# Performance work log

Measured on AMD Instinct MI355X. Metric: run time of the kernel, lower is better.

The kernel has to match this reference:

```python
import jax, jax.numpy as jnp
import numpy as np

N_EDGES = 1_600_000
N_NODES = 100_000
IN_CH = 32
OUT_CH = 64
TOTAL_DIM = IN_CH * 4 * 3  # 4 aggregators x 3 scalers


def setup_inputs() -> dict:
    key = jax.random.key(0)
    k1, k2, k3, k4 = jax.random.split(key, 4)
    messages = jax.random.normal(k1, (N_EDGES, IN_CH), dtype=jnp.float32)
    dst = jax.random.randint(k2, (N_EDGES,), 0, N_NODES, dtype=jnp.int64)
    W = jax.random.normal(k3, (OUT_CH, TOTAL_DIM), dtype=jnp.float32) / np.sqrt(TOTAL_DIM)
    b = jax.random.normal(k4, (OUT_CH,), dtype=jnp.float32) * 0.01
    return {"messages": messages, "dst": dst, "num_nodes": N_NODES, "W": W, "b": b}


def reference(messages, dst, num_nodes, W, b):
    # degree (clamped to >=1, matching scatter_count)
    ones = jnp.ones(dst.shape[0], dtype=messages.dtype)
    deg_raw = jax.ops.segment_sum(ones, dst, num_segments=num_nodes)
    deg = jnp.maximum(deg_raw, 1.0)

    # mean
    s = jax.ops.segment_sum(messages, dst, num_segments=num_nodes)  # [N, d]
    mean = s / deg[:, None]

    # max / min with empty-segment -> 0 (torch fills -inf/+inf then zeroes)
    mx = jax.ops.segment_max(messages, dst, num_segments=num_nodes)
    mx = jnp.where(jnp.isneginf(mx), jnp.zeros_like(mx), mx)
    mn = jax.ops.segment_min(messages, dst, num_segments=num_nodes)
    mn = jnp.where(jnp.isposinf(mn), jnp.zeros_like(mn), mn)

    # std: mean of squared deviations from per-node mean
    sq_diff = (messages - mean[dst]) ** 2
    var = jax.ops.segment_sum(sq_diff, dst, num_segments=num_nodes) / deg[:, None]
    std = jnp.sqrt(var + 1e-8)

    amp = jnp.log(deg + 1.0)[:, None]       # amplification scaler
    att = (1.0 / (deg + 1.0))[:, None]      # attenuation scaler

    results = []
    for agg in (mean, mx, mn, std):  # order matches default aggregators
        results.extend([agg, agg * amp, agg * att])  # identity, amp, att
    combined = jnp.concatenate(results, axis=-1)  # [N, 12*d]
    return combined @ W.T + b
```

## Files before the change

kernel.cpp:

```cpp
#include <hip/hip_runtime.h>
#include <math.h>

#define NE 1600000
#define NN 100000
#define NBKT 391
#define BINCH 8192
#define NBINBLK ((NE + BINCH - 1) / BINCH)

typedef __attribute__((ext_vector_type(8))) short bf16x8;
typedef __attribute__((ext_vector_type(4))) float f32x4;

static __device__ inline short f2bf(float f) {
  unsigned u = __float_as_uint(f);
  u += 0x7FFFu + ((u >> 16) & 1u);
  return (short)(u >> 16);
}

__global__ void k_init0(int* __restrict__ bktcnt) {
  int t = threadIdx.x;
  if (t < NBKT) bktcnt[t] = 0;
}

__global__ void k_wprep(const float* __restrict__ W, short* __restrict__ Wf) {
  int j = blockIdx.x * 256 + threadIdx.x;
  if (j < 12 * 4 * 64 * 8) {
    int i = j & 7, l = (j >> 3) & 63, ct = (j >> 9) & 3, kt = j >> 11;
    int col = ct * 16 + (l & 15);
    int k = kt * 32 + (l >> 4) * 8 + i;
    Wf[j] = f2bf(W[col * 384 + k]);
  }
}

__global__ __launch_bounds__(256) void k_bktcount(const int* __restrict__ dst,
                                                  int* __restrict__ bktcnt) {
  __shared__ int hist[NBKT];
  int t = threadIdx.x;
  for (int j = t; j < NBKT; j += 256) hist[j] = 0;
  __syncthreads();
  int start = blockIdx.x * BINCH;
  int lim = min(BINCH, NE - start);
  for (int j = t; j < lim; j += 256) atomicAdd(&hist[dst[start + j] >> 8], 1);
  __syncthreads();
  for (int j = t; j < NBKT; j += 256) {
    int h = hist[j];
    if (h) atomicAdd(&bktcnt[j], h);
  }
}

__global__ void k_bktscan(const int* __restrict__ bktcnt, int* __restrict__ bktoff,
                          int* __restrict__ bkcur, int* __restrict__ off) {
  __shared__ int s[512];
  int t = threadIdx.x;
  int v = (t < NBKT) ? bktcnt[t] : 0;
  s[t] = v;
  __syncthreads();
  for (int d = 1; d < 512; d <<= 1) {
    int x = (t >= d) ? s[t - d] : 0;
    __syncthreads();
    s[t] += x;
    __syncthreads();
  }
  if (t < NBKT) {
    int ex = s[t] - v;
    bktoff[t] = ex;
    bkcur[t] = ex;
  }
  if (t == 0) {
    bktoff[NBKT] = NE;
    off[NN] = NE;
  }
}

__global__ __launch_bounds__(256) void k_bin(const int* __restrict__ dst,
                                             int* __restrict__ bkcur,
                                             int2* __restrict__ pairs) {
  __shared__ int sdst[BINCH];
  __shared__ int hist[NBKT];
  int t = threadIdx.x;
  int start = blockIdx.x * BINCH;
  int lim = min(BINCH, NE - start);
  for (int j = t; j < NBKT; j += 256) hist[j] = 0;
  __syncthreads();
  for (int j = t; j < lim; j += 256) {
    int d = dst[start + j];
    sdst[j] = d;
    atomicAdd(&hist[d >> 8], 1);
  }
  __syncthreads();
  for (int j = t; j < NBKT; j += 256) {
    int h = hist[j];
    hist[j] = h ? atomicAdd(&bkcur[j], h) : 0;
  }
  __syncthreads();
  for (int j = t; j < lim; j += 256) {
    int d = sdst[j];
    int q = atomicAdd(&hist[d >> 8], 1);
    pairs[q] = make_int2(d, start + j);
  }
}

__global__ __launch_bounds__(256) void k_build(const int2* __restrict__ pairs,
                                               const int* __restrict__ bktoff,
                                               int* __restrict__ off,
                                               int* __restrict__ eid) {
  __shared__ int cnt[256];
  __shared__ int loc[256];
  int b = blockIdx.x, t = threadIdx.x;
  int base = bktoff[b];
  int m = bktoff[b + 1] - base;
  cnt[t] = 0;
  __syncthreads();
  for (int i = t; i < m; i += 256) atomicAdd(&cnt[pairs[base + i].x & 255], 1);
  __syncthreads();
  int v = cnt[t];
  loc[t] = v;
  __syncthreads();
  for (int d = 1; d < 256; d <<= 1) {
    int x = (t >= d) ? loc[t - d] : 0;
    __syncthreads();
    loc[t] += x;
    __syncthreads();
  }
  int ex = base + loc[t] - v;
  int node = b * 256 + t;
  if (node < NN) off[node] = ex;
  __syncthreads();
  loc[t] = ex;
  __syncthreads();
  for (int i = t; i < m; i += 256) {
    int2 pe = pairs[base + i];
    int p = atomicAdd(&loc[pe.x & 255], 1);
    eid[p] = pe.y;
  }
}

__global__ __launch_bounds__(256, 6) void k_fused(const float* __restrict__ msg,
                                                  const int* __restrict__ off,
                                                  const int* __restrict__ eid,
                                                  const short* __restrict__ Wf,
                                                  const float* __restrict__ bias,
                                                  float* __restrict__ out) {
  int wid = threadIdx.x >> 6, lane = threadIdx.x & 63;
  int r = lane & 15, oct = lane >> 4;
  int nb = (blockIdx.x * 4 + wid) * 16;
  if (nb >= NN) return;
  int node = nb + r;

  int e0 = off[node], e1 = off[node + 1];

  float sv[8], qv[8], xv[8], nv[8];
#pragma unroll
  for (int i = 0; i < 8; i++) {
    sv[i] = 0.f;
    qv[i] = 0.f;
    xv[i] = -INFINITY;
    nv[i] = INFINITY;
  }

  const float* mbase = msg + oct * 8;
  int p = e0;
  int nfull = (e1 - e0) >> 2;
  int ea0 = 0, ea1 = 0, ea2 = 0, ea3 = 0;
  if (nfull > 0) {
    ea0 = eid[p];
    ea1 = eid[p + 1];
    ea2 = eid[p + 2];
    ea3 = eid[p + 3];
  }
  for (int it = 0; it < nfull; ++it) {
    int c0 = ea0, c1 = ea1, c2 = ea2, c3 = ea3;
    p += 4;
    if (it + 1 < nfull) {
      ea0 = eid[p];
      ea1 = eid[p + 1];
      ea2 = eid[p + 2];
      ea3 = eid[p + 3];
    }
    const f32x4* r0 = (const f32x4*)(mbase + (size_t)c0 * 32);
    const f32x4* r1 = (const f32x4*)(mbase + (size_t)c1 * 32);
    const f32x4* r2 = (const f32x4*)(mbase + (size_t)c2 * 32);
    const f32x4* r3 = (const f32x4*)(mbase + (size_t)c3 * 32);
    f32x4 va0 = r0[0], vb0 = r0[1];
    f32x4 va1 = r1[0], vb1 = r1[1];
    f32x4 va2 = r2[0], vb2 = r2[1];
    f32x4 va3 = r3[0], vb3 = r3[1];
#pragma unroll
    for (int i = 0; i < 4; i++) {
      float w0 = va0[i], w1 = va1[i], w2 = va2[i], w3 = va3[i];
      sv[i] += w0 + w1 + w2 + w3;
      qv[i] += w0 * w0 + w1 * w1 + w2 * w2 + w3 * w3;
      xv[i] = fmaxf(fmaxf(xv[i], fmaxf(w0, w1)), fmaxf(w2, w3));
      nv[i] = fminf(fminf(nv[i], fminf(w0, w1)), fminf(w2, w3));
      float z0 = vb0[i], z1 = vb1[i], z2 = vb2[i], z3 = vb3[i];
      sv[i + 4] += z0 + z1 + z2 + z3;
      qv[i + 4] += z0 * z0 + z1 * z1 + z2 * z2 + z3 * z3;
      xv[i + 4] = fmaxf(fmaxf(xv[i + 4], fmaxf(z0, z1)), fmaxf(z2, z3));
      nv[i + 4] = fminf(fminf(nv[i + 4], fminf(z0, z1)), fminf(z2, z3));
    }
  }
  for (; p < e1; ++p) {
    int e = eid[p];
    const f32x4* rp = (const f32x4*)(mbase + (size_t)e * 32);
    f32x4 a = rp[0], b = rp[1];
#pragma unroll
    for (int i = 0; i < 4; i++) {
      float v0 = a[i], v1 = b[i];
      sv[i] += v0;
      qv[i] += v0 * v0;
      xv[i] = fmaxf(xv[i], v0);
      nv[i] = fminf(nv[i], v0);
      sv[i + 4] += v1;
      qv[i + 4] += v1 * v1;
      xv[i + 4] = fmaxf(xv[i + 4], v1);
      nv[i + 4] = fminf(nv[i + 4], v1);
    }
  }

  float degr = (float)(e1 - e0);
  float deg = fmaxf(degr, 1.f);
  float inv = 1.f / deg;
  float amp = logf(deg + 1.f);
  float att = 1.f / (deg + 1.f);

#pragma unroll
  for (int i = 0; i < 8; i++) {
    float me = sv[i] * inv;
    float va = fmaxf(qv[i] * inv - me * me, 0.f);
    sv[i] = me;
    qv[i] = sqrtf(va + 1e-8f);
    xv[i] = (xv[i] == -INFINITY) ? 0.f : xv[i];
    nv[i] = (nv[i] == INFINITY) ? 0.f : nv[i];
  }

  f32x4 acc[4] = {{0.f, 0.f, 0.f, 0.f},
                  {0.f, 0.f, 0.f, 0.f},
                  {0.f, 0.f, 0.f, 0.f},
                  {0.f, 0.f, 0.f, 0.f}};
  float scal[3] = {1.f, amp, att};
  const bf16x8* Bp = (const bf16x8*)Wf;
#pragma unroll
  for (int kt = 0; kt < 12; kt++) {
    const float* ag = (kt < 3) ? sv : (kt < 6) ? xv : (kt < 9) ? nv : qv;
    float sc = scal[kt % 3];
    bf16x8 b0 = Bp[(kt * 4 + 0) * 64 + lane];
    bf16x8 b1 = Bp[(kt * 4 + 1) * 64 + lane];
    bf16x8 b2 = Bp[(kt * 4 + 2) * 64 + lane];
    bf16x8 b3 = Bp[(kt * 4 + 3) * 64 + lane];
    bf16x8 af;
#pragma unroll
    for (int i = 0; i < 8; i++) af[i] = f2bf(ag[i] * sc);
    acc[0] = __builtin_amdgcn_mfma_f32_16x16x32_bf16(af, b0, acc[0], 0, 0, 0);
    acc[1] = __builtin_amdgcn_mfma_f32_16x16x32_bf16(af, b1, acc[1], 0, 0, 0);
    acc[2] = __builtin_amdgcn_mfma_f32_16x16x32_bf16(af, b2, acc[2], 0, 0, 0);
    acc[3] = __builtin_amdgcn_mfma_f32_16x16x32_bf16(af, b3, acc[3], 0, 0, 0);
    __builtin_amdgcn_sched_barrier(0);
  }

#pragma unroll
  for (int ct = 0; ct < 4; ct++) {
    int ocol = ct * 16 + r;
    float bb = bias[ocol];
#pragma unroll
    for (int j = 0; j < 4; j++) {
      int orow = nb + oct * 4 + j;
      out[orow * 64 + ocol] = acc[ct][j] + bb;
    }
  }
}

extern "C" void kernel_launch(void* const* d_in, const int* in_sizes, int n_in,
                              void* d_out, int out_size, void* d_ws, size_t ws_size,
                              hipStream_t stream) {
  const float* msg = (const float*)d_in[0];
  const int* dst = (const int*)d_in[1];
  const float* W = (const float*)d_in[3];
  const float* bias = (const float*)d_in[4];
  float* out = (float*)d_out;

  int* wsi = (int*)d_ws;
  int2* pairs = (int2*)wsi;
  int* eid = wsi + 2 * NE;
  int* off = wsi + 3 * NE;
  int* bktcnt = wsi + 3 * NE + NN + 1;
  int* bktoff = bktcnt + NBKT;
  int* bkcur = bktoff + NBKT + 1;
  short* Wfrag = (short*)(bkcur + NBKT);

  k_init0<<<1, 512, 0, stream>>>(bktcnt);
  k_wprep<<<96, 256, 0, stream>>>(W, Wfrag);
  k_bktcount<<<NBINBLK, 256, 0, stream>>>(dst, bktcnt);
  k_bktscan<<<1, 512, 0, stream>>>(bktcnt, bktoff, bkcur, off);
  k_bin<<<NBINBLK, 256, 0, stream>>>(dst, bkcur, pairs);
  k_build<<<NBKT, 256, 0, stream>>>(pairs, bktoff, off, eid);
  k_fused<<<(NN / 16 + 3) / 4, 256, 0, stream>>>(msg, off, eid, Wfrag, bias, out);
}
```

Measured before the change: 128.5 us.

## Permute messages into a per-node contiguous bf16 buffer before aggregation

Adds a new path, used when the workspace is large enough. It builds CSR offsets with per-node atomic counting and a two-pass scan. It then scatters every message row into a destination-sorted buffer packed as bf16, so the fused aggregation kernel streams contiguous rows instead of gathering through an edge-id indirection. This is meant to remove the random-gather latency and the eid loads in the fused kernel. In exchange it adds a full write and re-read of a 100MB permuted copy with scattered writes, and it rounds messages to bf16 before computing the mean, std, max and min. The old bucket-sort path is kept as a fallback for small workspaces.

```diff
diff --git a/kernel.cpp b/kernel.cpp
--- a/kernel.cpp
+++ b/kernel.cpp
@@ -3,12 +3,14 @@
 
 #define NE 1600000
 #define NN 100000
+#define NBLK ((NN + 255) / 256)
 #define NBKT 391
 #define BINCH 8192
 #define NBINBLK ((NE + BINCH - 1) / BINCH)
 
 typedef __attribute__((ext_vector_type(8))) short bf16x8;
 typedef __attribute__((ext_vector_type(4))) float f32x4;
+typedef __attribute__((ext_vector_type(4))) unsigned int u32x4;
 
 static __device__ inline short f2bf(float f) {
   unsigned u = __float_as_uint(f);
@@ -16,10 +18,11 @@
   return (short)(u >> 16);
 }
 
-__global__ void k_init0(int* __restrict__ bktcnt) {
-  int t = threadIdx.x;
-  if (t < NBKT) bktcnt[t] = 0;
-}
+static __device__ inline void unpack2(unsigned int u, float& lo, float& hi) {
+  lo = __uint_as_float(u << 16);
+  hi = __uint_as_float(u & 0xffff0000u);
+}
+
 
 __global__ void k_wprep(const float* __restrict__ W, short* __restrict__ Wf) {
   int j = blockIdx.x * 256 + threadIdx.x;
@@ -29,6 +32,209 @@
     int k = kt * 32 + (l >> 4) * 8 + i;
     Wf[j] = f2bf(W[col * 384 + k]);
   }
+}
+
+__global__ void k_zero(int* __restrict__ cnt) {
+  int i = blockIdx.x * 256 + threadIdx.x;
+  if (i < NN) cnt[i] = 0;
+}
+
+__global__ void k_count(const int* __restrict__ dst, int* __restrict__ cnt) {
+  int e = (blockIdx.x * 256 + threadIdx.x) * 4;
+  if (e + 4 <= NE) {
+    int4 d4 = *(const int4*)(dst + e);
+    atomicAdd(&cnt[d4.x], 1);
+    atomicAdd(&cnt[d4.y], 1);
+    atomicAdd(&cnt[d4.z], 1);
+    atomicAdd(&cnt[d4.w], 1);
+  } else {
+    for (; e < NE; ++e) atomicAdd(&cnt[dst[e]], 1);
+  }
+}
+
+__global__ void k_scan1(const int* __restrict__ cnt, int* __restrict__ bsum) {
+  __shared__ int s[256];
+  int t = threadIdx.x, i = blockIdx.x * 256 + t;
+  s[t] = (i < NN) ? cnt[i] : 0;
+  __syncthreads();
+  for (int d = 128; d > 0; d >>= 1) {
+    if (t < d) s[t] += s[t + d];
+    __syncthreads();
+  }
+  if (t == 0) bsum[blockIdx.x] = s[0];
+}
+
+__global__ void k_scan3(const int* __restrict__ cnt, const int* __restrict__ bsum,
+                        int* __restrict__ off, int* __restrict__ cur) {
+  __shared__ int pre[256];
+  __shared__ int s[256];
+  int t = threadIdx.x, b = blockIdx.x, i = b * 256 + t;
+  int a = 0;
+  for (int j = t; j < b; j += 256) a += bsum[j];
+  pre[t] = a;
+  __syncthreads();
+  for (int d = 128; d > 0; d >>= 1) {
+    if (t < d) pre[t] += pre[t + d];
+    __syncthreads();
+  }
+  int base = pre[0];
+  int v = (i < NN) ? cnt[i] : 0;
+  s[t] = v;
+  __syncthreads();
+  for (int d = 1; d < 256; d <<= 1) {
+    int x = (t >= d) ? s[t - d] : 0;
+    __syncthreads();
+    s[t] += x;
+    __syncthreads();
+  }
+  int ex = s[t] - v + base;
+  if (i < NN) {
+    off[i] = ex;
+    cur[i] = ex;
+  }
+  if (i == NN - 1) off[NN] = ex + v;
+}
+
+
+__global__ __launch_bounds__(256) void k_perm(const float* __restrict__ msg,
+                                              const int* __restrict__ dst,
+                                              int* __restrict__ cur,
+                                              unsigned int* __restrict__ pm) {
+  int gid = blockIdx.x * 256 + threadIdx.x;
+  int e = gid >> 3, q = gid & 7;
+  f32x4 v = *(const f32x4*)(msg + (size_t)gid * 4);
+  int lane = threadIdx.x & 63;
+  int p = 0;
+  if ((lane & 7) == 0) p = atomicAdd(&cur[dst[e]], 1);
+  p = __shfl(p, lane & 56);
+  unsigned int u0 =
+      (unsigned int)(unsigned short)f2bf(v[0]) | ((unsigned int)(unsigned short)f2bf(v[1]) << 16);
+  unsigned int u1 =
+      (unsigned int)(unsigned short)f2bf(v[2]) | ((unsigned int)(unsigned short)f2bf(v[3]) << 16);
+  *(uint2*)((char*)pm + (size_t)p * 64 + q * 8) = make_uint2(u0, u1);
+}
+
+__global__ __launch_bounds__(256, 6) void k_fused(const unsigned int* __restrict__ pm,
+                                                  const int* __restrict__ off,
+                                                  const short* __restrict__ Wf,
+                                                  const float* __restrict__ bias,
+                                                  float* __restrict__ out) {
+  int wid = threadIdx.x >> 6, lane = threadIdx.x & 63;
+  int r = lane & 15, oct = lane >> 4;
+  int nb = (blockIdx.x * 4 + wid) * 16;
+  if (nb >= NN) return;
+  int node = nb + r;
+
+  int e0 = off[node], e1 = off[node + 1];
+
+  float sv[8], qv[8], xv[8], nv[8];
+#pragma unroll
+  for (int i = 0; i < 8; i++) {
+    sv[i] = 0.f;
+    qv[i] = 0.f;
+    xv[i] = -INFINITY;
+    nv[i] = INFINITY;
+  }
+
+  int p = e0;
+  int nfull = (e1 - e0) >> 2;
+  for (int it = 0; it < nfull; ++it, p += 4) {
+    u32x4 U0 = *(const u32x4*)(pm + (size_t)p * 16 + oct * 4);
+    u32x4 U1 = *(const u32x4*)(pm + (size_t)(p + 1) * 16 + oct * 4);
+    u32x4 U2 = *(const u32x4*)(pm + (size_t)(p + 2) * 16 + oct * 4);
+    u32x4 U3 = *(const u32x4*)(pm + (size_t)(p + 3) * 16 + oct * 4);
+#pragma unroll
+    for (int j = 0; j < 4; j++) {
+      float a0, b0, a1, b1, a2, b2, a3, b3;
+      unpack2(U0[j], a0, b0);
+      unpack2(U1[j], a1, b1);
+      unpack2(U2[j], a2, b2);
+      unpack2(U3[j], a3, b3);
+      int i0 = 2 * j, i1 = 2 * j + 1;
+      sv[i0] += a0 + a1 + a2 + a3;
+      qv[i0] += a0 * a0 + a1 * a1 + a2 * a2 + a3 * a3;
+      xv[i0] = fmaxf(fmaxf(xv[i0], fmaxf(a0, a1)), fmaxf(a2, a3));
+      nv[i0] = fminf(fminf(nv[i0], fminf(a0, a1)), fminf(a2, a3));
+      sv[i1] += b0 + b1 + b2 + b3;
+      qv[i1] += b0 * b0 + b1 * b1 + b2 * b2 + b3 * b3;
+      xv[i1] = fmaxf(fmaxf(xv[i1], fmaxf(b0, b1)), fmaxf(b2, b3));
+      nv[i1] = fminf(fminf(nv[i1], fminf(b0, b1)), fminf(b2, b3));
+    }
+  }
+  for (; p < e1; ++p) {
+    u32x4 U = *(const u32x4*)(pm + (size_t)p * 16 + oct * 4);
+#pragma unroll
+    for (int j = 0; j < 4; j++) {
+      float a, b;
+      unpack2(U[j], a, b);
+      int i0 = 2 * j, i1 = 2 * j + 1;
+      sv[i0] += a;
+      qv[i0] += a * a;
+      xv[i0] = fmaxf(xv[i0], a);
+      nv[i0] = fminf(nv[i0], a);
+      sv[i1] += b;
+      qv[i1] += b * b;
+      xv[i1] = fmaxf(xv[i1], b);
+      nv[i1] = fminf(nv[i1], b);
+    }
+  }
+
+  float degr = (float)(e1 - e0);
+  float deg = fmaxf(degr, 1.f);
+  float inv = 1.f / deg;
+  float amp = logf(deg + 1.f);
+  float att = 1.f / (deg + 1.f);
+
+#pragma unroll
+  for (int i = 0; i < 8; i++) {
+    float me = sv[i] * inv;
+    float va = fmaxf(qv[i] * inv - me * me, 0.f);
+    sv[i] = me;
+    qv[i] = sqrtf(va + 1e-8f);
+    xv[i] = (xv[i] == -INFINITY) ? 0.f : xv[i];
+    nv[i] = (nv[i] == INFINITY) ? 0.f : nv[i];
+  }
+
+  f32x4 acc[4] = {{0.f, 0.f, 0.f, 0.f},
+                  {0.f, 0.f, 0.f, 0.f},
+                  {0.f, 0.f, 0.f, 0.f},
+                  {0.f, 0.f, 0.f, 0.f}};
+  float scal[3] = {1.f, amp, att};
+  const bf16x8* Bp = (const bf16x8*)Wf;
+#pragma unroll
+  for (int kt = 0; kt < 12; kt++) {
+    const float* ag = (kt < 3) ? sv : (kt < 6) ? xv : (kt < 9) ? nv : qv;
+    float sc = scal[kt % 3];
+    bf16x8 b0 = Bp[(kt * 4 + 0) * 64 + lane];
+    bf16x8 b1 = Bp[(kt * 4 + 1) * 64 + lane];
+    bf16x8 b2 = Bp[(kt * 4 + 2) * 64 + lane];
+    bf16x8 b3 = Bp[(kt * 4 + 3) * 64 + lane];
+    bf16x8 af;
+#pragma unroll
+    for (int i = 0; i < 8; i++) af[i] = f2bf(ag[i] * sc);
+    acc[0] = __builtin_amdgcn_mfma_f32_16x16x32_bf16(af, b0, acc[0], 0, 0, 0);
+    acc[1] = __builtin_amdgcn_mfma_f32_16x16x32_bf16(af, b1, acc[1], 0, 0, 0);
+    acc[2] = __builtin_amdgcn_mfma_f32_16x16x32_bf16(af, b2, acc[2], 0, 0, 0);
+    acc[3] = __builtin_amdgcn_mfma_f32_16x16x32_bf16(af, b3, acc[3], 0, 0, 0);
+    __builtin_amdgcn_sched_barrier(0);
+  }
+
+#pragma unroll
+  for (int ct = 0; ct < 4; ct++) {
+    int ocol = ct * 16 + r;
+    float bb = bias[ocol];
+#pragma unroll
+    for (int j = 0; j < 4; j++) {
+      int orow = nb + oct * 4 + j;
+      out[orow * 64 + ocol] = acc[ct][j] + bb;
+    }
+  }
+}
+
+
+__global__ void k_init0(int* __restrict__ bktcnt) {
+  int t = threadIdx.x;
+  if (t < NBKT) bktcnt[t] = 0;
 }
 
 __global__ __launch_bounds__(256) void k_bktcount(const int* __restrict__ dst,
@@ -129,17 +335,17 @@
   __syncthreads();
   for (int i = t; i < m; i += 256) {
     int2 pe = pairs[base + i];
-    int p = atomicAdd(&loc[pe.x & 255], 1);
-    eid[p] = pe.y;
-  }
-}
-
-__global__ __launch_bounds__(256, 6) void k_fused(const float* __restrict__ msg,
-                                                  const int* __restrict__ off,
-                                                  const int* __restrict__ eid,
-                                                  const short* __restrict__ Wf,
-                                                  const float* __restrict__ bias,
-                                                  float* __restrict__ out) {
+    int pdst = atomicAdd(&loc[pe.x & 255], 1);
+    eid[pdst] = pe.y;
+  }
+}
+
+__global__ __launch_bounds__(256, 6) void k_fusedg(const float* __restrict__ msg,
+                                                   const int* __restrict__ off,
+                                                   const int* __restrict__ eid,
+                                                   const short* __restrict__ Wf,
+                                                   const float* __restrict__ bias,
+                                                   float* __restrict__ out) {
   int wid = threadIdx.x >> 6, lane = threadIdx.x & 63;
   int r = lane & 15, oct = lane >> 4;
   int nb = (blockIdx.x * 4 + wid) * 16;
@@ -158,47 +364,7 @@
   }
 
   const float* mbase = msg + oct * 8;
-  int p = e0;
-  int nfull = (e1 - e0) >> 2;
-  int ea0 = 0, ea1 = 0, ea2 = 0, ea3 = 0;
-  if (nfull > 0) {
-    ea0 = eid[p];
-    ea1 = eid[p + 1];
-    ea2 = eid[p + 2];
-    ea3 = eid[p + 3];
-  }
-  for (int it = 0; it < nfull; ++it) {
-    int c0 = ea0, c1 = ea1, c2 = ea2, c3 = ea3;
-    p += 4;
-    if (it + 1 < nfull) {
-      ea0 = eid[p];
-      ea1 = eid[p + 1];
-      ea2 = eid[p + 2];
-      ea3 = eid[p + 3];
-    }
-    const f32x4* r0 = (const f32x4*)(mbase + (size_t)c0 * 32);
-    const f32x4* r1 = (const f32x4*)(mbase + (size_t)c1 * 32);
-    const f32x4* r2 = (const f32x4*)(mbase + (size_t)c2 * 32);
-    const f32x4* r3 = (const f32x4*)(mbase + (size_t)c3 * 32);
-    f32x4 va0 = r0[0], vb0 = r0[1];
-    f32x4 va1 = r1[0], vb1 = r1[1];
-    f32x4 va2 = r2[0], vb2 = r2[1];
-    f32x4 va3 = r3[0], vb3 = r3[1];
-#pragma unroll
-    for (int i = 0; i < 4; i++) {
-      float w0 = va0[i], w1 = va1[i], w2 = va2[i], w3 = va3[i];
-      sv[i] += w0 + w1 + w2 + w3;
-      qv[i] += w0 * w0 + w1 * w1 + w2 * w2 + w3 * w3;
-      xv[i] = fmaxf(fmaxf(xv[i], fmaxf(w0, w1)), fmaxf(w2, w3));
-      nv[i] = fminf(fminf(nv[i], fminf(w0, w1)), fminf(w2, w3));
-      float z0 = vb0[i], z1 = vb1[i], z2 = vb2[i], z3 = vb3[i];
-      sv[i + 4] += z0 + z1 + z2 + z3;
-      qv[i + 4] += z0 * z0 + z1 * z1 + z2 * z2 + z3 * z3;
-      xv[i + 4] = fmaxf(fmaxf(xv[i + 4], fmaxf(z0, z1)), fmaxf(z2, z3));
-      nv[i + 4] = fminf(fminf(nv[i + 4], fminf(z0, z1)), fminf(z2, z3));
-    }
-  }
-  for (; p < e1; ++p) {
+  for (int p = e0; p < e1; ++p) {
     int e = eid[p];
     const f32x4* rp = (const f32x4*)(mbase + (size_t)e * 32);
     f32x4 a = rp[0], b = rp[1];
@@ -268,6 +434,7 @@
   }
 }
 
+
 extern "C" void kernel_launch(void* const* d_in, const int* in_sizes, int n_in,
                               void* d_out, int out_size, void* d_ws, size_t ws_size,
                               hipStream_t stream) {
@@ -277,20 +444,39 @@
   const float* bias = (const float*)d_in[4];
   float* out = (float*)d_out;
 
-  int* wsi = (int*)d_ws;
-  int2* pairs = (int2*)wsi;
-  int* eid = wsi + 2 * NE;
-  int* off = wsi + 3 * NE;
-  int* bktcnt = wsi + 3 * NE + NN + 1;
-  int* bktoff = bktcnt + NBKT;
-  int* bkcur = bktoff + NBKT + 1;
-  short* Wfrag = (short*)(bkcur + NBKT);
-
-  k_init0<<<1, 512, 0, stream>>>(bktcnt);
-  k_wprep<<<96, 256, 0, stream>>>(W, Wfrag);
-  k_bktcount<<<NBINBLK, 256, 0, stream>>>(dst, bktcnt);
-  k_bktscan<<<1, 512, 0, stream>>>(bktcnt, bktoff, bkcur, off);
-  k_bin<<<NBINBLK, 256, 0, stream>>>(dst, bkcur, pairs);
-  k_build<<<NBKT, 256, 0, stream>>>(pairs, bktoff, off, eid);
-  k_fused<<<(NN / 16 + 3) / 4, 256, 0, stream>>>(msg, off, eid, Wfrag, bias, out);
-}
+  const size_t NEWWS = (size_t)NE * 64 + (size_t)(3 * NN + 1 + NBLK) * 4 + (size_t)24576 * 2;
+
+  if (ws_size >= NEWWS) {
+    unsigned int* pm = (unsigned int*)d_ws;
+    int* cnt = (int*)(pm + (size_t)NE * 16);
+    int* off = cnt + NN;
+    int* cur = off + NN + 1;
+    int* bsum = cur + NN;
+    short* Wfrag = (short*)(bsum + NBLK);
+
+    k_wprep<<<96, 256, 0, stream>>>(W, Wfrag);
+    k_zero<<<NBLK, 256, 0, stream>>>(cnt);
+    k_count<<<(NE / 4 + 255) / 256, 256, 0, stream>>>(dst, cnt);
+    k_scan1<<<NBLK, 256, 0, stream>>>(cnt, bsum);
+    k_scan3<<<NBLK, 256, 0, stream>>>(cnt, bsum, off, cur);
+    k_perm<<<NE * 8 / 256, 256, 0, stream>>>(msg, dst, cur, pm);
+    k_fused<<<(NN / 16 + 3) / 4, 256, 0, stream>>>(pm, off, Wfrag, bias, out);
+  } else {
+    int* wsi = (int*)d_ws;
+    int2* pairs = (int2*)wsi;
+    int* eid = wsi + 2 * NE;
+    int* off = wsi + 3 * NE;
+    int* bktcnt = wsi + 3 * NE + NN + 1;
+    int* bktoff = bktcnt + NBKT;
+    int* bkcur = bktoff + NBKT + 1;
+    short* Wfrag = (short*)(bkcur + NBKT);
+
+    k_init0<<<1, 512, 0, stream>>>(bktcnt);
+    k_wprep<<<96, 256, 0, stream>>>(W, Wfrag);
+    k_bktcount<<<NBINBLK, 256, 0, stream>>>(dst, bktcnt);
+    k_bktscan<<<1, 512, 0, stream>>>(bktcnt, bktoff, bkcur, off);
+    k_bin<<<NBINBLK, 256, 0, stream>>>(dst, bkcur, pairs);
+    k_build<<<NBKT, 256, 0, stream>>>(pairs, bktoff, off, eid);
+    k_fusedg<<<(NN / 16 + 3) / 4, 256, 0, stream>>>(msg, off, eid, Wfrag, bias, out);
+  }
+}
```

Result: slower. 201.7 us (+57.0%).

## Scatter bf16-packed message payloads into bucket order during binning

Applied to the files above, without the earlier changes.

The binning pass now also reads each message row, converts it to bf16, and writes it into a bucket-sorted payload array alongside the destination. The fused aggregation kernel then gathers 64-byte bf16 rows that are roughly locality-sorted, instead of random 128-byte fp32 rows. This halves the gather bytes and improves locality, at the cost of an extra full pass writing the payload during binning. It also lowers precision of the statistics (sum, sumsq, max, min) to bf16 inputs.

```diff
diff --git a/kernel.cpp b/kernel.cpp
--- a/kernel.cpp
+++ b/kernel.cpp
@@ -4,11 +4,13 @@
 #define NE 1600000
 #define NN 100000
 #define NBKT 391
-#define BINCH 8192
-#define NBINBLK ((NE + BINCH - 1) / BINCH)
+#define PCH 6250
+#define CBIN 8192
+#define NCBLK ((NE + CBIN - 1) / CBIN)
 
 typedef __attribute__((ext_vector_type(8))) short bf16x8;
 typedef __attribute__((ext_vector_type(4))) float f32x4;
+typedef __attribute__((ext_vector_type(4))) unsigned int u32x4;
 
 static __device__ inline short f2bf(float f) {
   unsigned u = __float_as_uint(f);
@@ -16,9 +18,13 @@
   return (short)(u >> 16);
 }
 
-__global__ void k_init0(int* __restrict__ bktcnt) {
-  int t = threadIdx.x;
-  if (t < NBKT) bktcnt[t] = 0;
+static __device__ inline unsigned int pack2(float a, float b) {
+  return (unsigned int)(unsigned short)f2bf(a) | ((unsigned int)(unsigned short)f2bf(b) << 16);
+}
+
+static __device__ inline void unpack2(unsigned int u, float& lo, float& hi) {
+  lo = __uint_as_float(u << 16);
+  hi = __uint_as_float(u & 0xffff0000u);
 }
 
 __global__ void k_wprep(const float* __restrict__ W, short* __restrict__ Wf) {
@@ -31,14 +37,19 @@
   }
 }
 
+__global__ void k_zerob(int* __restrict__ bktcnt) {
+  int t = threadIdx.x;
+  if (t < NBKT) bktcnt[t] = 0;
+}
+
 __global__ __launch_bounds__(256) void k_bktcount(const int* __restrict__ dst,
                                                   int* __restrict__ bktcnt) {
   __shared__ int hist[NBKT];
   int t = threadIdx.x;
   for (int j = t; j < NBKT; j += 256) hist[j] = 0;
   __syncthreads();
-  int start = blockIdx.x * BINCH;
-  int lim = min(BINCH, NE - start);
+  int start = blockIdx.x * CBIN;
+  int lim = min(CBIN, NE - start);
   for (int j = t; j < lim; j += 256) atomicAdd(&hist[dst[start + j] >> 8], 1);
   __syncthreads();
   for (int j = t; j < NBKT; j += 256) {
@@ -71,35 +82,44 @@
   }
 }
 
-__global__ __launch_bounds__(256) void k_bin(const int* __restrict__ dst,
-                                             int* __restrict__ bkcur,
-                                             int2* __restrict__ pairs) {
-  __shared__ int sdst[BINCH];
+__global__ __launch_bounds__(768) void k_binpay(const float* __restrict__ msg,
+                                                const int* __restrict__ dst,
+                                                int* __restrict__ bkcur,
+                                                unsigned int* __restrict__ pay,
+                                                int* __restrict__ pdst) {
+  __shared__ int sdst[PCH];
   __shared__ int hist[NBKT];
   int t = threadIdx.x;
-  int start = blockIdx.x * BINCH;
-  int lim = min(BINCH, NE - start);
-  for (int j = t; j < NBKT; j += 256) hist[j] = 0;
-  __syncthreads();
-  for (int j = t; j < lim; j += 256) {
+  int start = blockIdx.x * PCH;
+  for (int j = t; j < NBKT; j += 768) hist[j] = 0;
+  __syncthreads();
+  for (int j = t; j < PCH; j += 768) {
     int d = dst[start + j];
     sdst[j] = d;
     atomicAdd(&hist[d >> 8], 1);
   }
   __syncthreads();
-  for (int j = t; j < NBKT; j += 256) {
+  for (int j = t; j < NBKT; j += 768) {
     int h = hist[j];
     hist[j] = h ? atomicAdd(&bkcur[j], h) : 0;
   }
   __syncthreads();
-  for (int j = t; j < lim; j += 256) {
-    int d = sdst[j];
-    int q = atomicAdd(&hist[d >> 8], 1);
-    pairs[q] = make_int2(d, start + j);
-  }
-}
-
-__global__ __launch_bounds__(256) void k_build(const int2* __restrict__ pairs,
+  int qt = t & 7;
+  int lane = t & 63;
+  for (int eb = t >> 3; eb < PCH; eb += 96) {
+    int n = sdst[eb];
+    int q = 0;
+    if (qt == 0) q = atomicAdd(&hist[n >> 8], 1);
+    q = __shfl(q, lane & 56);
+    f32x4 v = *(const f32x4*)(msg + (size_t)(start + eb) * 32 + qt * 4);
+    unsigned int u0 = pack2(v[0], v[1]);
+    unsigned int u1 = pack2(v[2], v[3]);
+    *(uint2*)(pay + (size_t)q * 16 + qt * 2) = make_uint2(u0, u1);
+    if (qt == 0) pdst[q] = n;
+  }
+}
+
+__global__ __launch_bounds__(256) void k_build(const int* __restrict__ pdst,
                                                const int* __restrict__ bktoff,
                                                int* __restrict__ off,
                                                int* __restrict__ eid) {
@@ -110,7 +130,7 @@
   int m = bktoff[b + 1] - base;
   cnt[t] = 0;
   __syncthreads();
-  for (int i = t; i < m; i += 256) atomicAdd(&cnt[pairs[base + i].x & 255], 1);
+  for (int i = t; i < m; i += 256) atomicAdd(&cnt[pdst[base + i] & 255], 1);
   __syncthreads();
   int v = cnt[t];
   loc[t] = v;
@@ -128,18 +148,18 @@
   loc[t] = ex;
   __syncthreads();
   for (int i = t; i < m; i += 256) {
-    int2 pe = pairs[base + i];
-    int p = atomicAdd(&loc[pe.x & 255], 1);
-    eid[p] = pe.y;
-  }
-}
-
-__global__ __launch_bounds__(256, 6) void k_fused(const float* __restrict__ msg,
-                                                  const int* __restrict__ off,
-                                                  const int* __restrict__ eid,
-                                                  const short* __restrict__ Wf,
-                                                  const float* __restrict__ bias,
-                                                  float* __restrict__ out) {
+    int n = pdst[base + i];
+    int p = atomicAdd(&loc[n & 255], 1);
+    eid[p] = base + i;
+  }
+}
+
+__global__ __launch_bounds__(256, 6) void k_fusedS(const unsigned int* __restrict__ pay,
+                                                   const int* __restrict__ off,
+                                                   const int* __restrict__ eid,
+                                                   const short* __restrict__ Wf,
+                                                   const float* __restrict__ bias,
+                                                   float* __restrict__ out) {
   int wid = threadIdx.x >> 6, lane = threadIdx.x & 63;
   int r = lane & 15, oct = lane >> 4;
   int nb = (blockIdx.x * 4 + wid) * 16;
@@ -157,7 +177,6 @@
     nv[i] = INFINITY;
   }
 
-  const float* mbase = msg + oct * 8;
   int p = e0;
   int nfull = (e1 - e0) >> 2;
   int ea0 = 0, ea1 = 0, ea2 = 0, ea3 = 0;
@@ -176,43 +195,44 @@
       ea2 = eid[p + 2];
       ea3 = eid[p + 3];
     }
-    const f32x4* r0 = (const f32x4*)(mbase + (size_t)c0 * 32);
-    const f32x4* r1 = (const f32x4*)(mbase + (size_t)c1 * 32);
-    const f32x4* r2 = (const f32x4*)(mbase + (size_t)c2 * 32);
-    const f32x4* r3 = (const f32x4*)(mbase + (size_t)c3 * 32);
-    f32x4 va0 = r0[0], vb0 = r0[1];
-    f32x4 va1 = r1[0], vb1 = r1[1];
-    f32x4 va2 = r2[0], vb2 = r2[1];
-    f32x4 va3 = r3[0], vb3 = r3[1];
-#pragma unroll
-    for (int i = 0; i < 4; i++) {
-      float w0 = va0[i], w1 = va1[i], w2 = va2[i], w3 = va3[i];
-      sv[i] += w0 + w1 + w2 + w3;
-      qv[i] += w0 * w0 + w1 * w1 + w2 * w2 + w3 * w3;
-      xv[i] = fmaxf(fmaxf(xv[i], fmaxf(w0, w1)), fmaxf(w2, w3));
-      nv[i] = fminf(fminf(nv[i], fminf(w0, w1)), fminf(w2, w3));
-      float z0 = vb0[i], z1 = vb1[i], z2 = vb2[i], z3 = vb3[i];
-      sv[i + 4] += z0 + z1 + z2 + z3;
-      qv[i + 4] += z0 * z0 + z1 * z1 + z2 * z2 + z3 * z3;
-      xv[i + 4] = fmaxf(fmaxf(xv[i + 4], fmaxf(z0, z1)), fmaxf(z2, z3));
-      nv[i + 4] = fminf(fminf(nv[i + 4], fminf(z0, z1)), fminf(z2, z3));
+    u32x4 U0 = *(const u32x4*)(pay + (size_t)c0 * 16 + oct * 4);
+    u32x4 U1 = *(const u32x4*)(pay + (size_t)c1 * 16 + oct * 4);
+    u32x4 U2 = *(const u32x4*)(pay + (size_t)c2 * 16 + oct * 4);
+    u32x4 U3 = *(const u32x4*)(pay + (size_t)c3 * 16 + oct * 4);
+#pragma unroll
+    for (int j = 0; j < 4; j++) {
+      float a0, b0, a1, b1, a2, b2, a3, b3;
+      unpack2(U0[j], a0, b0);
+      unpack2(U1[j], a1, b1);
+      unpack2(U2[j], a2, b2);
+      unpack2(U3[j], a3, b3);
+      int i0 = 2 * j, i1 = 2 * j + 1;
+      sv[i0] += a0 + a1 + a2 + a3;
+      qv[i0] += a0 * a0 + a1 * a1 + a2 * a2 + a3 * a3;
+      xv[i0] = fmaxf(fmaxf(xv[i0], fmaxf(a0, a1)), fmaxf(a2, a3));
+      nv[i0] = fminf(fminf(nv[i0], fminf(a0, a1)), fminf(a2, a3));
+      sv[i1] += b0 + b1 + b2 + b3;
+      qv[i1] += b0 * b0 + b1 * b1 + b2 * b2 + b3 * b3;
+      xv[i1] = fmaxf(fmaxf(xv[i1], fmaxf(b0, b1)), fmaxf(b2, b3));
+      nv[i1] = fminf(fminf(nv[i1], fminf(b0, b1)), fminf(b2, b3));
     }
   }
   for (; p < e1; ++p) {
     int e = eid[p];
-    const f32x4* rp = (const f32x4*)(mbase + (size_t)e * 32);
-    f32x4 a = rp[0], b = rp[1];
-#pragma unroll
-    for (int i = 0; i < 4; i++) {
-      float v0 = a[i], v1 = b[i];
-      sv[i] += v0;
-      qv[i] += v0 * v0;
-      xv[i] = fmaxf(xv[i], v0);
-      nv[i] = fminf(nv[i], v0);
-      sv[i + 4] += v1;
-      qv[i + 4] += v1 * v1;
-      xv[i + 4] = fmaxf(xv[i + 4], v1);
-      nv[i + 4] = fminf(nv[i + 4], v1);
+    u32x4 U = *(const u32x4*)(pay + (size_t)e * 16 + oct * 4);
+#pragma unroll
+    for (int j = 0; j < 4; j++) {
+      float a, b;
+      unpack2(U[j], a, b);
+      int i0 = 2 * j, i1 = 2 * j + 1;
+      sv[i0] += a;
+      qv[i0] += a * a;
+      xv[i0] = fmaxf(xv[i0], a);
+      nv[i0] = fminf(nv[i0], a);
+      sv[i1] += b;
+      qv[i1] += b * b;
+      xv[i1] = fmaxf(xv[i1], b);
+      nv[i1] = fminf(nv[i1], b);
     }
   }
 
@@ -277,20 +297,20 @@
   const float* bias = (const float*)d_in[4];
   float* out = (float*)d_out;
 
-  int* wsi = (int*)d_ws;
-  int2* pairs = (int2*)wsi;
-  int* eid = wsi + 2 * NE;
-  int* off = wsi + 3 * NE;
-  int* bktcnt = wsi + 3 * NE + NN + 1;
+  unsigned int* pay = (unsigned int*)d_ws;
+  int* pdst = (int*)(pay + (size_t)NE * 16);
+  int* eid = pdst + NE;
+  int* off = eid + NE;
+  int* bktcnt = off + NN + 1;
   int* bktoff = bktcnt + NBKT;
   int* bkcur = bktoff + NBKT + 1;
   short* Wfrag = (short*)(bkcur + NBKT);
 
-  k_init0<<<1, 512, 0, stream>>>(bktcnt);
   k_wprep<<<96, 256, 0, stream>>>(W, Wfrag);
-  k_bktcount<<<NBINBLK, 256, 0, stream>>>(dst, bktcnt);
+  k_zerob<<<1, 512, 0, stream>>>(bktcnt);
+  k_bktcount<<<NCBLK, 256, 0, stream>>>(dst, bktcnt);
   k_bktscan<<<1, 512, 0, stream>>>(bktcnt, bktoff, bkcur, off);
-  k_bin<<<NBINBLK, 256, 0, stream>>>(dst, bkcur, pairs);
-  k_build<<<NBKT, 256, 0, stream>>>(pairs, bktoff, off, eid);
-  k_fused<<<(NN / 16 + 3) / 4, 256, 0, stream>>>(msg, off, eid, Wfrag, bias, out);
-}
+  k_binpay<<<256, 768, 0, stream>>>(msg, dst, bkcur, pay, pdst);
+  k_build<<<NBKT, 256, 0, stream>>>(pdst, bktoff, off, eid);
+  k_fusedS<<<(NN / 16 + 3) / 4, 256, 0, stream>>>(pay, off, eid, Wfrag, bias, out);
+}
```

Result: slower. 176.8 us (+37.6%).
